# Performance work log

Hardware: AMD Instinct MI355X
Metric: run time of the kernel (lower is better)

## Reference

```python
import jax, jax.numpy as jnp
import numpy as np

H, DK, DV = 16, 128, 128
BINS = 64
EPS = 1e-6
NORM_EPS = 1e-5


def silu(x):
    return x * jax.nn.sigmoid(x)


def short_conv(x, w):
    # causal depthwise conv over time + silu. x: [B,T,C], w: [C,K]
    C = x.shape[-1]
    K = w.shape[1]
    lhs = jnp.swapaxes(x, 1, 2)              # [B,C,T]
    rhs = w[:, None, :]                      # [C,1,K]
    out = jax.lax.conv_general_dilated(
        lhs, rhs, window_strides=(1,), padding=[(K - 1, 0)],
        dimension_numbers=('NCH', 'OIH', 'NCH'), feature_group_count=C)
    return silu(jnp.swapaxes(out, 1, 2))


def delta_rule(q, k, v, beta, decay):
    # gated delta-rule linear attention recurrence.
    # q,k: [B,T,H,DK], v: [B,T,H,DV], beta: [B,T,H], decay: [B,T,H,DK]
    B = q.shape[0]

    def step(S, inp):
        qt, kt, vt, bt, gt = inp             # [B,H,DK],...,[B,H],[B,H,DK]
        Sd = S * gt[..., None]               # per-key-channel decay
        v_pred = jnp.einsum('bhk,bhkv->bhv', kt, Sd)
        S_new = Sd + jnp.einsum('bhk,bhv->bhkv', kt * bt[..., None], vt - v_pred)
        ot = jnp.einsum('bhk,bhkv->bhv', qt, S_new)
        return S_new, ot

    tm = lambda a: jnp.swapaxes(a, 0, 1)     # time-major
    S0 = jnp.zeros((B, H, DK, DV), q.dtype)
    _, o = jax.lax.scan(step, S0, (tm(q), tm(k), tm(v), tm(beta), tm(decay)))
    return jnp.swapaxes(o, 0, 1)             # [B,T,H,DV]


def _forward(hidden_states, wq, wk, wv, conv_q_w, conv_k_w, conv_v_w, A_log, dt_bias,
             proxy_w, unc_w, head_embed, mlp_w1, mlp_b1, mlp_w2, mlp_b2,
             bb_w, bb_b, bd_w, bd_b, lam_w, lam_b, ab_w, ab_b, ad_w, ad_b,
             g1_w, g2_w, g2_b, onorm_w, wo):
    x = hidden_states
    B, T, _ = x.shape
    q = short_conv(x @ wq, conv_q_w).reshape(B, T, H, DK)
    k = short_conv(x @ wk, conv_k_w).reshape(B, T, H, DK)
    v = short_conv(x @ wv, conv_v_w).reshape(B, T, H, DV)

    # uncertainty (entropy of predicted-token distribution proxy)
    logp = jax.nn.log_softmax(x @ unc_w, axis=-1)
    entropy = -jnp.sum(jnp.exp(logp) * logp, axis=-1)              # [B,T]
    ent_norm = entropy / jnp.log(jnp.asarray(BINS, x.dtype))

    # beta-norm: unit-norm keys inside the kernel
    k_unit = k / (jnp.linalg.norm(k, axis=-1, keepdims=True) + EPS)

    # proxy-value surprise features, per head/token
    v_hat = jnp.einsum('bthk,kv->bthv', k, proxy_w)
    err = v - v_hat
    err_n = jnp.linalg.norm(err, axis=-1)                          # [B,T,H]
    v_n = jnp.linalg.norm(v, axis=-1)
    vh_n = jnp.linalg.norm(v_hat, axis=-1)
    rel_err = err_n / (v_n + EPS)
    cos = jnp.sum(v * v_hat, axis=-1) / (v_n * vh_n + EPS)
    feats = jnp.stack([jnp.broadcast_to(ent_norm[..., None], err_n.shape),
                       rel_err, cos, jnp.log1p(err_n)], axis=-1)    # [B,T,H,4]
    he = jnp.broadcast_to(head_embed[None, None], (B, T, H, head_embed.shape[-1]))
    feats = jnp.concatenate([feats, he], axis=-1)                   # [B,T,H,8]

    hf = silu(silu(feats @ mlp_w1 + mlp_b1) @ mlp_w2 + mlp_b2)      # [B,T,H,32]
    beta_base = hf @ bb_w + bb_b[0]
    beta_delta = hf @ bd_w + bd_b[0]
    beta_fast = jax.nn.sigmoid(beta_base + beta_delta)              # fast memory: bigger step
    beta_slow = jax.nn.sigmoid(beta_base - beta_delta)              # slow memory: smaller step
    lam = jax.nn.sigmoid(hf @ lam_w + lam_b[0])                     # mixing gate
    amp_base = hf @ ab_w + ab_b[0]
    amp_delta = hf @ ad_w + ad_b[0]
    amp_fast = jax.nn.sigmoid(amp_base + amp_delta)
    amp_slow = jax.nn.sigmoid(amp_base - amp_delta)

    # KDA-style per-key-channel log-decay: g = -exp(A_log) * softplus(dt_bias)
    g_chan = -jnp.exp(A_log)[:, None] * jax.nn.softplus(dt_bias).reshape(H, DK)
    decay_fast = jnp.exp(g_chan[None, None] * amp_fast[..., None])  # [B,T,H,DK]
    decay_slow = jnp.exp(g_chan[None, None] * amp_slow[..., None])

    qs = q * (DK ** -0.5)
    o_fast = delta_rule(qs, k_unit, v, beta_fast, decay_fast)
    o_slow = delta_rule(qs, k_unit, v, beta_slow, decay_slow)
    o = lam[..., None] * o_fast + (1.0 - lam[..., None]) * o_slow   # [B,T,H,DV]

    # gated RMSNorm (sigmoid gate) + output projection
    g = ((x @ g1_w) @ g2_w + g2_b).reshape(B, T, H, DV)
    rms = jnp.sqrt(jnp.mean(o * o, axis=-1, keepdims=True) + NORM_EPS)
    o = (o / rms) * onorm_w * jax.nn.sigmoid(g)
    return o.reshape(B, T, H * DV) @ wo


def setup_inputs() -> dict:
    key = jax.random.key(0)
    ks = jax.random.split(key, 40)
    B, T, D = 2, 256, 2048

    def w(k, shape, fan_in):
        return jax.random.normal(k, shape, jnp.float32) * (fan_in ** -0.5)

    return {
        'hidden_states': jax.random.normal(ks[0], (B, T, D), jnp.float32),
        'wq': w(ks[1], (D, H * DK), D),
        'wk': w(ks[2], (D, H * DK), D),
        'wv': w(ks[3], (D, H * DV), D),
        'conv_q_w': w(ks[4], (H * DK, 4), 4),
        'conv_k_w': w(ks[5], (H * DK, 4), 4),
        'conv_v_w': w(ks[6], (H * DV, 4), 4),
        'A_log': jnp.log(jax.random.uniform(ks[7], (H,), jnp.float32, 1.0, 16.0)),
        'dt_bias': jnp.zeros((H * DK,), jnp.float32),
        'proxy_w': w(ks[8], (DK, DV), DK),
        'unc_w': w(ks[9], (D, BINS), D),
        'head_embed': jax.random.normal(ks[10], (H, 4), jnp.float32),
        'mlp_w1': w(ks[11], (8, 32), 8),
        'mlp_b1': jnp.zeros((32,), jnp.float32),
        'mlp_w2': w(ks[12], (32, 32), 32),
        'mlp_b2': jnp.zeros((32,), jnp.float32),
        'bb_w': w(ks[13], (32,), 32), 'bb_b': jnp.zeros((1,), jnp.float32),
        'bd_w': w(ks[14], (32,), 32), 'bd_b': jnp.zeros((1,), jnp.float32),
        'lam_w': w(ks[15], (32,), 32), 'lam_b': jnp.zeros((1,), jnp.float32),
        'ab_w': w(ks[16], (32,), 32), 'ab_b': jnp.zeros((1,), jnp.float32),
        'ad_w': w(ks[17], (32,), 32), 'ad_b': jnp.zeros((1,), jnp.float32),
        'g1_w': w(ks[18], (D, DV), D),
        'g2_w': w(ks[19], (DV, H * DV), DV),
        'g2_b': jnp.zeros((H * DV,), jnp.float32),
        'onorm_w': jnp.ones((DV,), jnp.float32),
        'wo': w(ks[20], (H * DV, D), H * DV),
    }


def reference(hidden_states, wq, wk, wv, conv_q_w, conv_k_w, conv_v_w, A_log, dt_bias,
              proxy_w, unc_w, head_embed, mlp_w1, mlp_b1, mlp_w2, mlp_b2,
              bb_w, bb_b, bd_w, bd_b, lam_w, lam_b, ab_w, ab_b, ad_w, ad_b,
              g1_w, g2_w, g2_b, onorm_w, wo):
    return _forward(hidden_states, wq, wk, wv, conv_q_w, conv_k_w, conv_v_w, A_log,
                    dt_bias, proxy_w, unc_w, head_embed, mlp_w1, mlp_b1, mlp_w2, mlp_b2,
                    bb_w, bb_b, bd_w, bd_b, lam_w, lam_b, ab_w, ab_b, ad_w, ad_b,
                    g1_w, g2_w, g2_b, onorm_w, wo)
```

## Files before the change

kernel.cpp:

```cpp
#include <hip/hip_runtime.h>
#include <hip/hip_bf16.h>
#include <math.h>

#define H_ 16
#define DK_ 128
#define DV_ 128
#define D_ 2048
#define T_ 256
#define B_ 2
#define BT_ 512

typedef __attribute__((ext_vector_type(8))) short short8v;
typedef __attribute__((ext_vector_type(4))) float float4v;
typedef unsigned short ushort_t;

__device__ __forceinline__ float sigmoidf_(float x){ return 1.f/(1.f+expf(-x)); }
__device__ __forceinline__ float siluf_(float x){ return x/(1.f+expf(-x)); }
__device__ __forceinline__ ushort_t f2bf(float f){
    __hip_bfloat16 h = __float2bfloat16(f);
    return *reinterpret_cast<ushort_t*>(&h);
}
__device__ __forceinline__ int swz(int row, int k){
    return row * 32 + ((((k >> 3) ^ (row & 3)) << 3) | (k & 7));
}

template<int CTRL>
__device__ __forceinline__ float ror_add_(float x){
    return x + __int_as_float(__builtin_amdgcn_update_dpp(
        0, __float_as_int(x), CTRL, 0xF, 0xF, true));
}
__device__ __forceinline__ float rsum16_(float x){
    x = ror_add_<0x121>(x);
    x = ror_add_<0x122>(x);
    x = ror_add_<0x124>(x);
    x = ror_add_<0x128>(x);
    return x;
}

__global__ void cvt_bf16(const float* __restrict__ in, ushort_t* __restrict__ out, int n){
    int i = (blockIdx.x * 256 + threadIdx.x) * 4;
    if (i >= n) return;
    float4 v = *(const float4*)&in[i];
    union { ushort_t s[4]; unsigned long long u; } p;
    p.s[0] = f2bf(v.x); p.s[1] = f2bf(v.y); p.s[2] = f2bf(v.z); p.s[3] = f2bf(v.w);
    *(unsigned long long*)&out[i] = p.u;
}

__global__ void cvt_strided(const float* __restrict__ Cb, ushort_t* __restrict__ out){
    int i = (blockIdx.x * 256 + threadIdx.x) * 4;
    int m = i >> 7, c = i & 127;
    float4 v = *(const float4*)&Cb[(size_t)m * 6336 + 6208 + c];
    union { ushort_t s[4]; unsigned long long u; } p;
    p.s[0] = f2bf(v.x); p.s[1] = f2bf(v.y); p.s[2] = f2bf(v.z); p.s[3] = f2bf(v.w);
    *(unsigned long long*)&out[i] = p.u;
}

__device__ __forceinline__ void gemm_core(
    const ushort_t* __restrict__ A, int K,
    const float* __restrict__ W, int Nst, int nloc0,
    float* __restrict__ C, int Cst, int m0, int n0out)
{
    __shared__ ushort_t Asub[2048];
    __shared__ ushort_t Bsub[2048];
    const int tid = threadIdx.x;
    const int wid = tid >> 6, lane = tid & 63;
    const int wr = (wid >> 1) * 32, wc = (wid & 1) * 32;
    const int lr = lane & 15, lk = (lane >> 4) * 8;
    const int rowA = tid >> 2, kqA = tid & 3;
    const int nW = tid & 63, kqW = tid >> 6;

    float4v acc[2][2];
    #pragma unroll
    for (int i = 0; i < 2; ++i)
        #pragma unroll
        for (int j = 0; j < 2; ++j) acc[i][j] = (float4v){0.f, 0.f, 0.f, 0.f};

    short8v aRa, aRb;
    float wRa[8], wRb[8];

#define LOADT(AR, WR, KOFF) do {                                                   \
    AR = *(const short8v*)&A[(size_t)(m0 + rowA) * K + (KOFF) + kqA * 8];          \
    _Pragma("unroll")                                                              \
    for (int r = 0; r < 8; ++r)                                                    \
        WR[r] = W[(size_t)((KOFF) + kqW * 8 + r) * Nst + nloc0 + nW];              \
} while (0)
#define STORET(AR, WR) do {                                                        \
    *(short8v*)&Asub[swz(rowA, kqA * 8)] = AR;                                     \
    union { ushort_t s[8]; short8v v; } pk;                                        \
    _Pragma("unroll")                                                              \
    for (int r = 0; r < 8; ++r) pk.s[r] = f2bf(WR[r]);                             \
    *(short8v*)&Bsub[swz(nW, kqW * 8)] = pk.v;                                     \
} while (0)
#define FRAGMMA() do {                                                             \
    short8v af0 = *(const short8v*)&Asub[swz(wr + lr, lk)];                        \
    short8v af1 = *(const short8v*)&Asub[swz(wr + 16 + lr, lk)];                   \
    short8v bf0 = *(const short8v*)&Bsub[swz(wc + lr, lk)];                        \
    short8v bf1 = *(const short8v*)&Bsub[swz(wc + 16 + lr, lk)];                   \
    acc[0][0] = __builtin_amdgcn_mfma_f32_16x16x32_bf16(af0, bf0, acc[0][0],0,0,0);\
    acc[0][1] = __builtin_amdgcn_mfma_f32_16x16x32_bf16(af0, bf1, acc[0][1],0,0,0);\
    acc[1][0] = __builtin_amdgcn_mfma_f32_16x16x32_bf16(af1, bf0, acc[1][0],0,0,0);\
    acc[1][1] = __builtin_amdgcn_mfma_f32_16x16x32_bf16(af1, bf1, acc[1][1],0,0,0);\
} while (0)

    LOADT(aRa, wRa, 0);
    for (int k0 = 0; k0 < K; k0 += 64) {
        STORET(aRa, wRa);
        __syncthreads();
        if (k0 + 32 < K) LOADT(aRb, wRb, k0 + 32);
        FRAGMMA();
        __syncthreads();
        STORET(aRb, wRb);
        __syncthreads();
        if (k0 + 64 < K) LOADT(aRa, wRa, k0 + 64);
        FRAGMMA();
        __syncthreads();
    }
#undef LOADT
#undef STORET
#undef FRAGMMA
    const int lq = (lane >> 4) * 4;
    #pragma unroll
    for (int mi = 0; mi < 2; ++mi)
        #pragma unroll
        for (int ni = 0; ni < 2; ++ni)
            #pragma unroll
            for (int j = 0; j < 4; ++j)
                C[(size_t)(m0 + wr + mi * 16 + lq + j) * Cst + (n0out + wc + ni * 16 + lr)]
                    = acc[mi][ni][j];
}

__device__ __forceinline__ void gemm_core2(
    const ushort_t* __restrict__ A, int K,
    const float* __restrict__ W, int Nst, int nloc0,
    float* __restrict__ C, int Cst, int m0, int n0out)
{
    __shared__ ushort_t Asub[8192];
    __shared__ ushort_t Bsub[2048];
    const int tid = threadIdx.x;
    const int wid = tid >> 6, lane = tid & 63;
    const int wr = wid * 32;
    const int lr = lane & 15, lk = (lane >> 4) * 8;
    const int rowA = tid >> 2;
    const int kqA  = (tid & 3) * 8;
    const int nW = tid & 63, kqW = (tid >> 6) & 3;
    const bool doW = tid < 256;

    float4v acc[2][4];
    #pragma unroll
    for (int i = 0; i < 2; ++i)
        #pragma unroll
        for (int j = 0; j < 4; ++j) acc[i][j] = (float4v){0.f, 0.f, 0.f, 0.f};

    short8v a0a, a1a, a0b, a1b;
    float wRa[8], wRb[8];

#define LOADT2(A0, A1, WR, KOFF) do {                                              \
    A0 = *(const short8v*)&A[(size_t)(m0 + rowA) * K + (KOFF) + kqA];              \
    A1 = *(const short8v*)&A[(size_t)(m0 + rowA + 128) * K + (KOFF) + kqA];        \
    if (doW) {                                                                     \
        _Pragma("unroll")                                                          \
        for (int r = 0; r < 8; ++r)                                                \
            WR[r] = W[(size_t)((KOFF) + kqW * 8 + r) * Nst + nloc0 + nW];          \
    }                                                                              \
} while (0)
#define STORET2(A0, A1, WR) do {                                                   \
    *(short8v*)&Asub[swz(rowA, kqA)] = A0;                                         \
    *(short8v*)&Asub[swz(rowA + 128, kqA)] = A1;                                   \
    if (doW) {                                                                     \
        union { ushort_t s[8]; short8v v; } pk;                                    \
        _Pragma("unroll")                                                          \
        for (int r = 0; r < 8; ++r) pk.s[r] = f2bf(WR[r]);                         \
        *(short8v*)&Bsub[swz(nW, kqW * 8)] = pk.v;                                 \
    }                                                                              \
} while (0)
#define FRAGMMA2() do {                                                            \
    short8v af0 = *(const short8v*)&Asub[swz(wr + lr, lk)];                        \
    short8v af1 = *(const short8v*)&Asub[swz(wr + 16 + lr, lk)];                   \
    short8v bf0 = *(const short8v*)&Bsub[swz(lr, lk)];                             \
    short8v bf1 = *(const short8v*)&Bsub[swz(16 + lr, lk)];                        \
    short8v bf2 = *(const short8v*)&Bsub[swz(32 + lr, lk)];                        \
    short8v bf3 = *(const short8v*)&Bsub[swz(48 + lr, lk)];                        \
    acc[0][0] = __builtin_amdgcn_mfma_f32_16x16x32_bf16(af0, bf0, acc[0][0],0,0,0);\
    acc[0][1] = __builtin_amdgcn_mfma_f32_16x16x32_bf16(af0, bf1, acc[0][1],0,0,0);\
    acc[0][2] = __builtin_amdgcn_mfma_f32_16x16x32_bf16(af0, bf2, acc[0][2],0,0,0);\
    acc[0][3] = __builtin_amdgcn_mfma_f32_16x16x32_bf16(af0, bf3, acc[0][3],0,0,0);\
    acc[1][0] = __builtin_amdgcn_mfma_f32_16x16x32_bf16(af1, bf0, acc[1][0],0,0,0);\
    acc[1][1] = __builtin_amdgcn_mfma_f32_16x16x32_bf16(af1, bf1, acc[1][1],0,0,0);\
    acc[1][2] = __builtin_amdgcn_mfma_f32_16x16x32_bf16(af1, bf2, acc[1][2],0,0,0);\
    acc[1][3] = __builtin_amdgcn_mfma_f32_16x16x32_bf16(af1, bf3, acc[1][3],0,0,0);\
} while (0)

    LOADT2(a0a, a1a, wRa, 0);
    for (int k0 = 0; k0 < K; k0 += 64) {
        STORET2(a0a, a1a, wRa);
        __syncthreads();
        if (k0 + 32 < K) LOADT2(a0b, a1b, wRb, k0 + 32);
        FRAGMMA2();
        __syncthreads();
        STORET2(a0b, a1b, wRb);
        __syncthreads();
        if (k0 + 64 < K) LOADT2(a0a, a1a, wRa, k0 + 64);
        FRAGMMA2();
        __syncthreads();
    }
#undef LOADT2
#undef STORET2
#undef FRAGMMA2
    const int lq = (lane >> 4) * 4;
    #pragma unroll
    for (int mi = 0; mi < 2; ++mi)
        #pragma unroll
        for (int ni = 0; ni < 4; ++ni)
            #pragma unroll
            for (int j = 0; j < 4; ++j)
                C[(size_t)(m0 + wr + mi * 16 + lq + j) * Cst + (n0out + ni * 16 + lr)]
                    = acc[mi][ni][j];
}

__global__ __launch_bounds__(512) void gemm_proj(const ushort_t* __restrict__ A,
    const float* __restrict__ wq, const float* __restrict__ wk, const float* __restrict__ wv,
    const float* __restrict__ unc, const float* __restrict__ g1, float* __restrict__ C)
{
    int n0 = blockIdx.x * 64, m0 = blockIdx.y * 256;
    const float* W; int nloc, Nst;
    if (n0 < 2048)      { W = wq;  nloc = n0;        Nst = 2048; }
    else if (n0 < 4096) { W = wk;  nloc = n0 - 2048; Nst = 2048; }
    else if (n0 < 6144) { W = wv;  nloc = n0 - 4096; Nst = 2048; }
    else if (n0 < 6208) { W = unc; nloc = n0 - 6144; Nst = 64; }
    else                { W = g1;  nloc = n0 - 6208; Nst = 128; }
    gemm_core2(A, 2048, W, Nst, nloc, C, 6336, m0, n0);
}

__global__ __launch_bounds__(256) void gemm_one(const ushort_t* __restrict__ A,
    const float* __restrict__ W, float* __restrict__ C, int N, int K)
{
    gemm_core(A, K, W, N, blockIdx.x * 64, C, N, blockIdx.y * 64, blockIdx.x * 64);
}

__global__ void conv_fused(const float* __restrict__ Cb,
    const float* __restrict__ wq, const float* __restrict__ wk, const float* __restrict__ wv,
    float* __restrict__ qc, float* __restrict__ kc, float* __restrict__ vc,
    ushort_t* __restrict__ kcb, float qscale)
{
    int c  = blockIdx.x * 256 + threadIdx.x;
    int bt = blockIdx.y;
    int b  = bt / T_, t = bt % T_;
    int which = c >> 11, cloc = c & 2047;
    const float* w = which == 0 ? wq : which == 1 ? wk : wv;
    float* o = which == 0 ? qc : which == 1 ? kc : vc;
    float scale = which == 0 ? qscale : 1.f;
    float acc = 0.f;
    #pragma unroll
    for (int j = 0; j < 4; ++j) {
        int tt = t - 3 + j;
        if (tt >= 0) acc = fmaf(w[cloc * 4 + j], Cb[((size_t)(b * T_ + tt)) * 6336 + c], acc);
    }
    float r = siluf_(acc) * scale;
    o[(size_t)bt * D_ + cloc] = r;
    if (which == 1) kcb[(size_t)bt * D_ + cloc] = f2bf(r);
}

__global__ void gchan_k(const float* __restrict__ A_log, const float* __restrict__ dt_bias,
                        float* __restrict__ gchan)
{
    int i = blockIdx.x * 256 + threadIdx.x;
    int h = i >> 7;
    float x = dt_bias[i];
    float sp = (x > 20.f) ? x : log1pf(expf(x));
    gchan[i] = -expf(A_log[h]) * sp * 1.44269504088896f;
}

__global__ __launch_bounds__(128) void feats_k(
    const float* __restrict__ kc, const float* __restrict__ vc,
    const float* __restrict__ vhatA, const float* __restrict__ Cb,
    const float* __restrict__ he,
    const float* __restrict__ w1, const float* __restrict__ b1,
    const float* __restrict__ w2, const float* __restrict__ b2,
    const float* __restrict__ bbw, const float* __restrict__ bbb,
    const float* __restrict__ bdw, const float* __restrict__ bdb,
    const float* __restrict__ lamw, const float* __restrict__ lamb,
    const float* __restrict__ abw, const float* __restrict__ abb,
    const float* __restrict__ adw, const float* __restrict__ adb,
    float* __restrict__ bf, float* __restrict__ bs, float* __restrict__ lm,
    float* __restrict__ af, float* __restrict__ as2, float* __restrict__ kn)
{
    int blk = blockIdx.x;
    int h = blk & 15, bt = blk >> 4;
    int b = bt / T_, t = bt % T_;
    int v = threadIdx.x;
    __shared__ float part[2][5];
    __shared__ float tot5[5];
    __shared__ float feats8[8];
    __shared__ float hf1[32];
    __shared__ float hf[32];
    __shared__ float entSh;

    if (v < 64) {
        float x = Cb[(size_t)bt * 6336 + 6144 + v];
        float m = x;
        #pragma unroll
        for (int o = 32; o > 0; o >>= 1) m = fmaxf(m, __shfl_xor(m, o));
        float e = expf(x - m);
        float s = e;
        #pragma unroll
        for (int o = 32; o > 0; o >>= 1) s += __shfl_xor(s, o);
        float lp = (x - m) - logf(s);
        float c = -expf(lp) * lp;
        #pragma unroll
        for (int o = 32; o > 0; o >>= 1) c += __shfl_xor(c, o);
        if (v == 0) entSh = c / logf(64.f);
    }

    size_t base = (size_t)bt * D_ + h * 128;
    float kval = kc[base + v];
    float vval = vc[base + v];
    float vhat = vhatA[(size_t)blk * 128 + v];

    float e = vval - vhat;
    float sums[5] = {kval * kval, vval * vval, vhat * vhat, vval * vhat, e * e};
    #pragma unroll
    for (int i = 0; i < 5; ++i) {
        float s = sums[i];
        #pragma unroll
        for (int o = 32; o > 0; o >>= 1) s += __shfl_xor(s, o);
        if ((threadIdx.x & 63) == 0) part[threadIdx.x >> 6][i] = s;
    }
    __syncthreads();
    if (threadIdx.x < 5) tot5[threadIdx.x] = part[0][threadIdx.x] + part[1][threadIdx.x];
    __syncthreads();
    if (threadIdx.x == 0) {
        float k2 = tot5[0], v2 = tot5[1], vh2 = tot5[2], vvh = tot5[3], e2 = tot5[4];
        float knorm = sqrtf(k2);
        float err_n = sqrtf(e2);
        float v_n = sqrtf(v2);
        float vh_n = sqrtf(vh2);
        feats8[0] = entSh;
        feats8[1] = err_n / (v_n + 1e-6f);
        feats8[2] = vvh / (v_n * vh_n + 1e-6f);
        feats8[3] = log1pf(err_n);
        feats8[4] = he[h * 4 + 0];
        feats8[5] = he[h * 4 + 1];
        feats8[6] = he[h * 4 + 2];
        feats8[7] = he[h * 4 + 3];
        kn[((size_t)(b * H_ + h)) * T_ + t] = knorm;
    }
    __syncthreads();
    if (threadIdx.x < 32) {
        float a = b1[threadIdx.x];
        #pragma unroll
        for (int j = 0; j < 8; ++j) a = fmaf(feats8[j], w1[j * 32 + threadIdx.x], a);
        hf1[threadIdx.x] = siluf_(a);
    }
    __syncthreads();
    if (threadIdx.x < 32) {
        float a = b2[threadIdx.x];
        #pragma unroll
        for (int j = 0; j < 32; ++j) a = fmaf(hf1[j], w2[j * 32 + threadIdx.x], a);
        hf[threadIdx.x] = siluf_(a);
    }
    __syncthreads();
    if (threadIdx.x == 0) {
        float bb = bbb[0], bd = bdb[0], lv = lamb[0], ab = abb[0], ad = adb[0];
        #pragma unroll
        for (int j = 0; j < 32; ++j) {
            float hj = hf[j];
            bb = fmaf(hj, bbw[j], bb);
            bd = fmaf(hj, bdw[j], bd);
            lv = fmaf(hj, lamw[j], lv);
            ab = fmaf(hj, abw[j], ab);
            ad = fmaf(hj, adw[j], ad);
        }
        size_t o = ((size_t)(b * H_ + h)) * T_ + t;
        bf[o]  = sigmoidf_(bb + bd);
        bs[o]  = sigmoidf_(bb - bd);
        lm[o]  = sigmoidf_(lv);
        af[o]  = sigmoidf_(ab + ad);
        as2[o] = sigmoidf_(ab - ad);
    }
}

__global__ __launch_bounds__(128) void precomp_k(
    const float* __restrict__ kc, const float* __restrict__ qc,
    const float* __restrict__ kn,
    const float* __restrict__ af, const float* __restrict__ as2,
    const float* __restrict__ bf, const float* __restrict__ bs,
    const float* __restrict__ gchan,
    float* __restrict__ kuA, float* __restrict__ dA, float4* __restrict__ scal4A)
{
    const int t = blockIdx.x;
    const int y = blockIdx.y;
    const int rule = y >> 5, b = (y >> 4) & 1, h = y & 15;
    const int k = threadIdx.x;
    const int sb = (b * 16 + h) * 256 + t;
    const float knv = kn[sb];
    const float am  = (rule ? as2 : af)[sb];
    const float btv = (rule ? bs : bf)[sb];
    const size_t idx = (size_t)(b * 256 + t) * D_ + h * 128 + k;
    const float kuv = kc[idx] / (knv + 1e-6f);
    if (rule == 0) kuA[((size_t)(b * 16 + h) * 256 + t) * 128 + k] = kuv;
    dA[((size_t)y * 256 + t) * 128 + k] = exp2f(gchan[h * 128 + k] * am);
    float p = qc[idx] * kuv;
    #pragma unroll
    for (int o = 32; o > 0; o >>= 1) p += __shfl_xor(p, o);
    __shared__ float pp[2];
    if ((k & 63) == 0) pp[k >> 6] = p;
    __syncthreads();
    if (k == 0) {
        float4 s; s.x = am; s.y = btv; s.z = (pp[0] + pp[1]) * btv; s.w = 0.f;
        scal4A[(size_t)y * 256 + t] = s;
    }
}

struct OPS { float4 a0, a1, q0, q1, d0, d1, sc; float2 vv; };

__global__ __launch_bounds__(256) void delta_wave9(
    const float* __restrict__ qc, const float* __restrict__ vc,
    const float* __restrict__ kuA, const float* __restrict__ dA,
    const float4* __restrict__ scal4A,
    float* __restrict__ o_fast, float* __restrict__ o_slow)
{
    const int p  = blockIdx.x;
    const int lb = (p & 7) * 32 + (p >> 3);
    const int bh = lb >> 3, rule = (lb >> 2) & 1, vq = lb & 3;
    const int b = bh >> 4, h = bh & 15;
    const int rbh = rule * 32 + bh;
    const int tid = threadIdx.x;
    const int wid = tid >> 6, lane = tid & 63;
    const int kl = lane & 15, vg = lane >> 4;
    const int vloc = wid * 8 + vg * 2;
    const int vcol = vq * 32 + vloc;

    __shared__ float kuL[2][16][144];
    __shared__ float qL [2][16][144];
    __shared__ float dL [2][16][144];
    __shared__ float vL [2][16][32];
    __shared__ float scL[2][16][4];

    const float*  __restrict__ pkuG = kuA + (size_t)bh * 256 * 128;
    const float*  __restrict__ pdG  = dA + (size_t)rbh * 256 * 128;
    const float*  __restrict__ pqG  = qc + (size_t)b * T_ * D_ + h * 128;
    const float*  __restrict__ pvG  = vc + (size_t)b * T_ * D_ + h * 128 + vq * 32;
    const float4* __restrict__ pscG = scal4A + (size_t)rbh * 256;
    float* __restrict__ obase = (rule ? o_slow : o_fast)
                                + (size_t)b * T_ * D_ + h * 128 + vcol;

    const int srow = (tid & 127) >> 3;
    const int scol = (tid & 7) * 16;
    const bool isK = tid < 128;
    const int ck0 = scol >> 3;
    const int fo_w0 = ck0 * 8 + (ck0 >> 2) * 4;
    const int fo_w1 = (ck0 + 1) * 8 + ((ck0 + 1) >> 2) * 4;

    float4 sb0, sb1, sb2, sb3, svb, ssc, sd0, sd1;

    float S[8][2];
    #pragma unroll
    for (int j = 0; j < 8; ++j) { S[j][0] = 0.f; S[j][1] = 0.f; }

#define STAGE_LOAD(C) do {                                                         \
    const int t0_ = (C) * 16;                                                      \
    const float* dsrc = pdG + (size_t)(t0_ + srow) * 128 + scol;                   \
    if (isK) {                                                                     \
        const float* src = pkuG + (size_t)(t0_ + srow) * 128 + scol;               \
        sb0 = *(const float4*)(src);      sb1 = *(const float4*)(src + 4);         \
        sb2 = *(const float4*)(src + 8);  sb3 = *(const float4*)(src + 12);        \
        svb = *(const float4*)(pvG + (size_t)(t0_ + srow) * D_ + (tid & 7) * 4);   \
        sd0 = *(const float4*)(dsrc);     sd1 = *(const float4*)(dsrc + 4);        \
    } else {                                                                       \
        const float* src = pqG + (size_t)(t0_ + srow) * D_ + scol;                 \
        sb0 = *(const float4*)(src);      sb1 = *(const float4*)(src + 4);         \
        sb2 = *(const float4*)(src + 8);  sb3 = *(const float4*)(src + 12);        \
        sd0 = *(const float4*)(dsrc + 8); sd1 = *(const float4*)(dsrc + 12);       \
        if ((tid & 127) < 16) ssc = *(const float4*)&pscG[t0_ + (tid & 127)];      \
    }                                                                              \
} while (0)

#define STAGE_WRITE(BI) do {                                                       \
    if (isK) {                                                                     \
        *(float4*)&kuL[BI][srow][fo_w0]     = sb0;                                 \
        *(float4*)&kuL[BI][srow][fo_w0 + 4] = sb1;                                 \
        *(float4*)&kuL[BI][srow][fo_w1]     = sb2;                                 \
        *(float4*)&kuL[BI][srow][fo_w1 + 4] = sb3;                                 \
        *(float4*)&vL[BI][srow][(tid & 7) * 4] = svb;                              \
        *(float4*)&dL[BI][srow][fo_w0]      = sd0;                                 \
        *(float4*)&dL[BI][srow][fo_w0 + 4]  = sd1;                                 \
    } else {                                                                       \
        *(float4*)&qL[BI][srow][fo_w0]     = sb0;                                  \
        *(float4*)&qL[BI][srow][fo_w0 + 4] = sb1;                                  \
        *(float4*)&qL[BI][srow][fo_w1]     = sb2;                                  \
        *(float4*)&qL[BI][srow][fo_w1 + 4] = sb3;                                  \
        *(float4*)&dL[BI][srow][fo_w1]      = sd0;                                 \
        *(float4*)&dL[BI][srow][fo_w1 + 4]  = sd1;                                 \
        if ((tid & 127) < 16) *(float4*)&scL[BI][tid & 127][0] = ssc;              \
    }                                                                              \
} while (0)

#define LDOPS(R, BI, TS) do {                                                      \
    R.a0 = *(const float4*)&kuL[BI][TS][fo];                                       \
    R.a1 = *(const float4*)&kuL[BI][TS][fo + 4];                                   \
    R.q0 = *(const float4*)&qL[BI][TS][fo];                                        \
    R.q1 = *(const float4*)&qL[BI][TS][fo + 4];                                    \
    R.d0 = *(const float4*)&dL[BI][TS][fo];                                        \
    R.d1 = *(const float4*)&dL[BI][TS][fo + 4];                                    \
    R.vv = *(const float2*)&vL[BI][TS][vloc];                                      \
    R.sc = *(const float4*)&scL[BI][TS][0];                                        \
} while (0)

#define STEP(TT, CUR, NXT, BI) do {                                                \
    if ((TT) + 1 < 16) LDOPS(NXT, BI, (TT) + 1);                                   \
    float ku[8] = {CUR.a0.x, CUR.a0.y, CUR.a0.z, CUR.a0.w,                         \
                   CUR.a1.x, CUR.a1.y, CUR.a1.z, CUR.a1.w};                        \
    float qv[8] = {CUR.q0.x, CUR.q0.y, CUR.q0.z, CUR.q0.w,                         \
                   CUR.q1.x, CUR.q1.y, CUR.q1.z, CUR.q1.w};                        \
    float d[8]  = {CUR.d0.x, CUR.d0.y, CUR.d0.z, CUR.d0.w,                         \
                   CUR.d1.x, CUR.d1.y, CUR.d1.z, CUR.d1.w};                        \
    float vp0a = 0.f, vp0b = 0.f, vp1a = 0.f, vp1b = 0.f;                          \
    float oq0a = 0.f, oq0b = 0.f, oq1a = 0.f, oq1b = 0.f;                          \
    _Pragma("unroll")                                                              \
    for (int j = 0; j < 4; ++j) {                                                  \
        float kudA = ku[j] * d[j],     qdA = qv[j] * d[j];                         \
        float kudB = ku[j+4] * d[j+4], qdB = qv[j+4] * d[j+4];                     \
        vp0a = fmaf(kudA, S[j][0], vp0a);   vp0b = fmaf(kudB, S[j+4][0], vp0b);    \
        vp1a = fmaf(kudA, S[j][1], vp1a);   vp1b = fmaf(kudB, S[j+4][1], vp1b);    \
        oq0a = fmaf(qdA,  S[j][0], oq0a);   oq0b = fmaf(qdB,  S[j+4][0], oq0b);    \
        oq1a = fmaf(qdA,  S[j][1], oq1a);   oq1b = fmaf(qdB,  S[j+4][1], oq1b);    \
    }                                                                              \
    float vp0 = rsum16_(vp0a + vp0b);                                              \
    float vp1 = rsum16_(vp1a + vp1b);                                              \
    float oq0 = rsum16_(oq0a + oq0b);                                              \
    float oq1 = rsum16_(oq1a + oq1b);                                              \
    float dv0 = CUR.vv.x - vp0, dv1 = CUR.vv.y - vp1;                              \
    float o0 = fmaf(CUR.sc.z, dv0, oq0);                                           \
    float o1 = fmaf(CUR.sc.z, dv1, oq1);                                           \
    float bd0 = CUR.sc.y * dv0, bd1 = CUR.sc.y * dv1;                              \
    _Pragma("unroll")                                                              \
    for (int j = 0; j < 8; ++j) {                                                  \
        S[j][0] = fmaf(d[j], S[j][0], ku[j] * bd0);                                \
        S[j][1] = fmaf(d[j], S[j][1], ku[j] * bd1);                                \
    }                                                                              \
    if (kl == 0) {                                                                 \
        float2 ov; ov.x = o0; ov.y = o1;                                           \
        *(float2*)&obase[(size_t)(tb + (TT)) * D_] = ov;                           \
    }                                                                              \
} while (0)

    const int fo = kl * 8 + (kl >> 2) * 4;

    STAGE_LOAD(0);
    STAGE_WRITE(0);
    __syncthreads();

    OPS rA, rB;
    for (int c = 0; c < 16; ++c) {
        if (c < 15) STAGE_LOAD(c + 1);
        const int bi = c & 1;
        const int tb = c * 16;
        LDOPS(rA, bi, 0);
        #pragma unroll
        for (int ts = 0; ts < 16; ts += 2) {
            STEP(ts,     rA, rB, bi);
            STEP(ts + 1, rB, rA, bi);
        }
        if (c < 15) STAGE_WRITE((c + 1) & 1);
        __syncthreads();
    }
#undef STAGE_LOAD
#undef STAGE_WRITE
#undef LDOPS
#undef STEP
}

__global__ __launch_bounds__(128) void combine_k(
    const float* __restrict__ of, const float* __restrict__ os,
    const float* __restrict__ lm, const float* __restrict__ graw,
    const float* __restrict__ g2b, const float* __restrict__ onw,
    ushort_t* __restrict__ ocb)
{
    int blk = blockIdx.x;
    int h = blk & 15, bt = blk >> 4;
    int b = bt / T_, t = bt % T_;
    int v = threadIdx.x;
    size_t idx = (size_t)bt * D_ + h * 128 + v;
    float l = lm[((size_t)(b * H_ + h)) * T_ + t];
    float o = l * of[idx] + (1.f - l) * os[idx];
    float s = o * o;
    #pragma unroll
    for (int off = 32; off > 0; off >>= 1) s += __shfl_xor(s, off);
    __shared__ float ws2[2];
    if ((threadIdx.x & 63) == 0) ws2[threadIdx.x >> 6] = s;
    __syncthreads();
    float tot = ws2[0] + ws2[1];
    float rms = sqrtf(tot / 128.f + 1e-5f);
    float g = graw[idx] + g2b[h * 128 + v];
    ocb[idx] = f2bf(o / rms * onw[v] * sigmoidf_(g));
}

extern "C" void kernel_launch(void* const* d_in, const int* in_sizes, int n_in,
                              void* d_out, int out_size, void* d_ws, size_t ws_size,
                              hipStream_t stream)
{
    const float* x        = (const float*)d_in[0];
    const float* wq       = (const float*)d_in[1];
    const float* wk       = (const float*)d_in[2];
    const float* wv       = (const float*)d_in[3];
    const float* conv_q_w = (const float*)d_in[4];
    const float* conv_k_w = (const float*)d_in[5];
    const float* conv_v_w = (const float*)d_in[6];
    const float* A_log    = (const float*)d_in[7];
    const float* dt_bias  = (const float*)d_in[8];
    const float* proxy_w  = (const float*)d_in[9];
    const float* unc_w    = (const float*)d_in[10];
    const float* he       = (const float*)d_in[11];
    const float* mlp_w1   = (const float*)d_in[12];
    const float* mlp_b1   = (const float*)d_in[13];
    const float* mlp_w2   = (const float*)d_in[14];
    const float* mlp_b2   = (const float*)d_in[15];
    const float* bb_w     = (const float*)d_in[16];
    const float* bb_b     = (const float*)d_in[17];
    const float* bd_w     = (const float*)d_in[18];
    const float* bd_b     = (const float*)d_in[19];
    const float* lam_w    = (const float*)d_in[20];
    const float* lam_b    = (const float*)d_in[21];
    const float* ab_w     = (const float*)d_in[22];
    const float* ab_b     = (const float*)d_in[23];
    const float* ad_w     = (const float*)d_in[24];
    const float* ad_b     = (const float*)d_in[25];
    const float* g1_w     = (const float*)d_in[26];
    const float* g2_w     = (const float*)d_in[27];
    const float* g2_b     = (const float*)d_in[28];
    const float* onorm_w  = (const float*)d_in[29];
    const float* wo       = (const float*)d_in[30];
    float* out = (float*)d_out;

    float* ws = (float*)d_ws;
    const size_t SZ = (size_t)BT_ * D_;
    float* C_big = ws;
    float* qc    = C_big + (size_t)512 * 6336;
    float* kc    = qc + SZ;
    float* vc    = kc + SZ;
    float* graw  = vc + SZ;
    float* bf    = graw + SZ;
    float* bs    = bf + 8192;
    float* lm    = bs + 8192;
    float* af    = lm + 8192;
    float* as2   = af + 8192;
    float* kn    = as2 + 8192;
    float* gchan = kn + 8192;
    float* scal4 = gchan + 2048;
    float* kuA   = scal4 + 65536;
    float* dA    = kuA + 1048576;
    float* fend  = dA + 2097152;
    ushort_t* xb    = (ushort_t*)fend;
    ushort_t* gtmpb = xb + SZ;

    float* o_fast  = C_big;
    float* o_slow  = C_big + SZ;
    ushort_t* ocb  = xb;
    float* vhatA   = kuA;
    ushort_t* kcb  = (ushort_t*)dA;

    dim3 blk256(256);
    dim3 blk512(512);
    const float QSCALE = 0.08838834764831845f;

    cvt_bf16<<<dim3(1024), blk256, 0, stream>>>(x, xb, (int)SZ);
    gemm_proj<<<dim3(99, 2), blk512, 0, stream>>>(xb, wq, wk, wv, unc_w, g1_w, C_big);
    cvt_strided<<<dim3(64), blk256, 0, stream>>>(C_big, gtmpb);
    gemm_one<<<dim3(32, 8), blk256, 0, stream>>>(gtmpb, g2_w, graw, 2048, 128);
    conv_fused<<<dim3(24, BT_), blk256, 0, stream>>>(C_big, conv_q_w, conv_k_w, conv_v_w,
                                                     qc, kc, vc, kcb, QSCALE);
    gemm_one<<<dim3(2, 128), blk256, 0, stream>>>(kcb, proxy_w, vhatA, 128, 128);
    gchan_k<<<dim3(8), blk256, 0, stream>>>(A_log, dt_bias, gchan);
    feats_k<<<dim3(BT_ * H_), dim3(128), 0, stream>>>(
        kc, vc, vhatA, C_big, he, mlp_w1, mlp_b1, mlp_w2, mlp_b2,
        bb_w, bb_b, bd_w, bd_b, lam_w, lam_b, ab_w, ab_b, ad_w, ad_b,
        bf, bs, lm, af, as2, kn);
    precomp_k<<<dim3(256, 64), dim3(128), 0, stream>>>(
        kc, qc, kn, af, as2, bf, bs, gchan, kuA, dA, (float4*)scal4);
    delta_wave9<<<dim3(256), blk256, 0, stream>>>(qc, vc, kuA, dA,
                                                  (const float4*)scal4,
                                                  o_fast, o_slow);
    combine_k<<<dim3(BT_ * H_), dim3(128), 0, stream>>>(o_fast, o_slow, lm, graw,
                                                        g2_b, onorm_w, ocb);
    gemm_one<<<dim3(32, 8), blk256, 0, stream>>>(ocb, wo, out, 2048, 2048);
}
```

Measured before the change: 219.1 us.

## Fuse feature, gate-channel and precompute kernels; fold g2 conversion into GEMM

Merges gchan_k, feats_k and precomp_k into one per-(token,head) kernel that computes the gating scalars in shared memory and directly writes kuA, both decay arrays and the scal4 entries. This drops the intermediate bf/bs/af/as2/kn buffers and two launches. The g2 GEMM now reads the fp32 slice of C_big and converts it to bf16 in its loader, which removes the cvt_strided pass. The output projection moves to the larger 512-thread gemm_core2 tile. In exchange, the merged kernel recomputes the softplus gate per block, and the bigger output tiles launch only 64 blocks.

```diff
diff --git a/kernel.cpp b/kernel.cpp
--- a/kernel.cpp
+++ b/kernel.cpp
@@ -41,15 +41,6 @@
     int i = (blockIdx.x * 256 + threadIdx.x) * 4;
     if (i >= n) return;
     float4 v = *(const float4*)&in[i];
-    union { ushort_t s[4]; unsigned long long u; } p;
-    p.s[0] = f2bf(v.x); p.s[1] = f2bf(v.y); p.s[2] = f2bf(v.z); p.s[3] = f2bf(v.w);
-    *(unsigned long long*)&out[i] = p.u;
-}
-
-__global__ void cvt_strided(const float* __restrict__ Cb, ushort_t* __restrict__ out){
-    int i = (blockIdx.x * 256 + threadIdx.x) * 4;
-    int m = i >> 7, c = i & 127;
-    float4 v = *(const float4*)&Cb[(size_t)m * 6336 + 6208 + c];
     union { ushort_t s[4]; unsigned long long u; } p;
     p.s[0] = f2bf(v.x); p.s[1] = f2bf(v.y); p.s[2] = f2bf(v.z); p.s[3] = f2bf(v.w);
     *(unsigned long long*)&out[i] = p.u;
@@ -237,6 +228,68 @@
     gemm_core(A, K, W, N, blockIdx.x * 64, C, N, blockIdx.y * 64, blockIdx.x * 64);
 }
 
+__global__ __launch_bounds__(512) void gemm_one2(const ushort_t* __restrict__ A,
+    const float* __restrict__ W, float* __restrict__ C, int N, int K)
+{
+    gemm_core2(A, K, W, N, blockIdx.x * 64, C, N, blockIdx.y * 256, blockIdx.x * 64);
+}
+
+__global__ __launch_bounds__(256) void gemm_g2(const float* __restrict__ Cb,
+    const float* __restrict__ W, float* __restrict__ C)
+{
+    __shared__ ushort_t Asub[2048];
+    __shared__ ushort_t Bsub[2048];
+    const int tid = threadIdx.x;
+    const int wid = tid >> 6, lane = tid & 63;
+    const int wr = (wid >> 1) * 32, wc = (wid & 1) * 32;
+    const int lr = lane & 15, lk = (lane >> 4) * 8;
+    const int rowA = tid >> 2, kqA = (tid & 3) * 8;
+    const int nW = tid & 63, kqW = tid >> 6;
+    const int m0 = blockIdx.y * 64, n0 = blockIdx.x * 64;
+
+    float4v acc[2][2];
+    #pragma unroll
+    for (int i = 0; i < 2; ++i)
+        #pragma unroll
+        for (int j = 0; j < 2; ++j) acc[i][j] = (float4v){0.f, 0.f, 0.f, 0.f};
+
+    for (int k0 = 0; k0 < 128; k0 += 32) {
+        const float* asrc = &Cb[(size_t)(m0 + rowA) * 6336 + 6208 + k0 + kqA];
+        float4 a4a = *(const float4*)asrc;
+        float4 a4b = *(const float4*)(asrc + 4);
+        float w8[8];
+        #pragma unroll
+        for (int r = 0; r < 8; ++r)
+            w8[r] = W[(size_t)(k0 + kqW * 8 + r) * 2048 + n0 + nW];
+        __syncthreads();
+        union { ushort_t s[8]; short8v v; } pa, pw;
+        pa.s[0]=f2bf(a4a.x); pa.s[1]=f2bf(a4a.y); pa.s[2]=f2bf(a4a.z); pa.s[3]=f2bf(a4a.w);
+        pa.s[4]=f2bf(a4b.x); pa.s[5]=f2bf(a4b.y); pa.s[6]=f2bf(a4b.z); pa.s[7]=f2bf(a4b.w);
+        *(short8v*)&Asub[swz(rowA, kqA)] = pa.v;
+        #pragma unroll
+        for (int r = 0; r < 8; ++r) pw.s[r] = f2bf(w8[r]);
+        *(short8v*)&Bsub[swz(nW, kqW * 8)] = pw.v;
+        __syncthreads();
+        short8v af0 = *(const short8v*)&Asub[swz(wr + lr, lk)];
+        short8v af1 = *(const short8v*)&Asub[swz(wr + 16 + lr, lk)];
+        short8v bf0 = *(const short8v*)&Bsub[swz(wc + lr, lk)];
+        short8v bf1 = *(const short8v*)&Bsub[swz(wc + 16 + lr, lk)];
+        acc[0][0] = __builtin_amdgcn_mfma_f32_16x16x32_bf16(af0, bf0, acc[0][0],0,0,0);
+        acc[0][1] = __builtin_amdgcn_mfma_f32_16x16x32_bf16(af0, bf1, acc[0][1],0,0,0);
+        acc[1][0] = __builtin_amdgcn_mfma_f32_16x16x32_bf16(af1, bf0, acc[1][0],0,0,0);
+        acc[1][1] = __builtin_amdgcn_mfma_f32_16x16x32_bf16(af1, bf1, acc[1][1],0,0,0);
+    }
+    const int lq = (lane >> 4) * 4;
+    #pragma unroll
+    for (int mi = 0; mi < 2; ++mi)
+        #pragma unroll
+        for (int ni = 0; ni < 2; ++ni)
+            #pragma unroll
+            for (int j = 0; j < 4; ++j)
+                C[(size_t)(m0 + wr + mi * 16 + lq + j) * 2048 + (n0 + wc + ni * 16 + lr)]
+                    = acc[mi][ni][j];
+}
+
 __global__ void conv_fused(const float* __restrict__ Cb,
     const float* __restrict__ wq, const float* __restrict__ wk, const float* __restrict__ wv,
     float* __restrict__ qc, float* __restrict__ kc, float* __restrict__ vc,
@@ -260,20 +313,12 @@
     if (which == 1) kcb[(size_t)bt * D_ + cloc] = f2bf(r);
 }
 
-__global__ void gchan_k(const float* __restrict__ A_log, const float* __restrict__ dt_bias,
-                        float* __restrict__ gchan)
-{
-    int i = blockIdx.x * 256 + threadIdx.x;
-    int h = i >> 7;
-    float x = dt_bias[i];
-    float sp = (x > 20.f) ? x : log1pf(expf(x));
-    gchan[i] = -expf(A_log[h]) * sp * 1.44269504088896f;
-}
-
-__global__ __launch_bounds__(128) void feats_k(
+__global__ __launch_bounds__(128) void featsprec_k(
     const float* __restrict__ kc, const float* __restrict__ vc,
+    const float* __restrict__ qc,
     const float* __restrict__ vhatA, const float* __restrict__ Cb,
     const float* __restrict__ he,
+    const float* __restrict__ A_log, const float* __restrict__ dt_bias,
     const float* __restrict__ w1, const float* __restrict__ b1,
     const float* __restrict__ w2, const float* __restrict__ b2,
     const float* __restrict__ bbw, const float* __restrict__ bbb,
@@ -281,8 +326,8 @@
     const float* __restrict__ lamw, const float* __restrict__ lamb,
     const float* __restrict__ abw, const float* __restrict__ abb,
     const float* __restrict__ adw, const float* __restrict__ adb,
-    float* __restrict__ bf, float* __restrict__ bs, float* __restrict__ lm,
-    float* __restrict__ af, float* __restrict__ as2, float* __restrict__ kn)
+    float* __restrict__ lm, float* __restrict__ kuA,
+    float* __restrict__ dA, float4* __restrict__ scal4A)
 {
     int blk = blockIdx.x;
     int h = blk & 15, bt = blk >> 4;
@@ -294,6 +339,7 @@
     __shared__ float hf1[32];
     __shared__ float hf[32];
     __shared__ float entSh;
+    __shared__ float scal5[5];
 
     if (v < 64) {
         float x = Cb[(size_t)bt * 6336 + 6144 + v];
@@ -342,7 +388,7 @@
         feats8[5] = he[h * 4 + 1];
         feats8[6] = he[h * 4 + 2];
         feats8[7] = he[h * 4 + 3];
-        kn[((size_t)(b * H_ + h)) * T_ + t] = knorm;
+        scal5[4] = knorm;
     }
     __syncthreads();
     if (threadIdx.x < 32) {
@@ -370,44 +416,36 @@
             ab = fmaf(hj, abw[j], ab);
             ad = fmaf(hj, adw[j], ad);
         }
-        size_t o = ((size_t)(b * H_ + h)) * T_ + t;
-        bf[o]  = sigmoidf_(bb + bd);
-        bs[o]  = sigmoidf_(bb - bd);
-        lm[o]  = sigmoidf_(lv);
-        af[o]  = sigmoidf_(ab + ad);
-        as2[o] = sigmoidf_(ab - ad);
-    }
-}
-
-__global__ __launch_bounds__(128) void precomp_k(
-    const float* __restrict__ kc, const float* __restrict__ qc,
-    const float* __restrict__ kn,
-    const float* __restrict__ af, const float* __restrict__ as2,
-    const float* __restrict__ bf, const float* __restrict__ bs,
-    const float* __restrict__ gchan,
-    float* __restrict__ kuA, float* __restrict__ dA, float4* __restrict__ scal4A)
-{
-    const int t = blockIdx.x;
-    const int y = blockIdx.y;
-    const int rule = y >> 5, b = (y >> 4) & 1, h = y & 15;
+        scal5[0] = sigmoidf_(bb + bd);
+        scal5[1] = sigmoidf_(bb - bd);
+        scal5[2] = sigmoidf_(ab + ad);
+        scal5[3] = sigmoidf_(ab - ad);
+        lm[((size_t)(b * H_ + h)) * T_ + t] = sigmoidf_(lv);
+    }
+    __syncthreads();
+
+    const float bfv = scal5[0], bsv = scal5[1];
+    const float afv = scal5[2], asv = scal5[3], knv = scal5[4];
     const int k = threadIdx.x;
-    const int sb = (b * 16 + h) * 256 + t;
-    const float knv = kn[sb];
-    const float am  = (rule ? as2 : af)[sb];
-    const float btv = (rule ? bs : bf)[sb];
-    const size_t idx = (size_t)(b * 256 + t) * D_ + h * 128 + k;
-    const float kuv = kc[idx] / (knv + 1e-6f);
-    if (rule == 0) kuA[((size_t)(b * 16 + h) * 256 + t) * 128 + k] = kuv;
-    dA[((size_t)y * 256 + t) * 128 + k] = exp2f(gchan[h * 128 + k] * am);
-    float p = qc[idx] * kuv;
-    #pragma unroll
-    for (int o = 32; o > 0; o >>= 1) p += __shfl_xor(p, o);
-    __shared__ float pp[2];
-    if ((k & 63) == 0) pp[k >> 6] = p;
-    __syncthreads();
-    if (k == 0) {
-        float4 s; s.x = am; s.y = btv; s.z = (pp[0] + pp[1]) * btv; s.w = 0.f;
-        scal4A[(size_t)y * 256 + t] = s;
+    const int bh = b * 16 + h;
+    float xdt = dt_bias[h * 128 + k];
+    float sp = (xdt > 20.f) ? xdt : log1pf(expf(xdt));
+    float gch = -expf(A_log[h]) * sp * 1.44269504088896f;
+    float kuv = kval / (knv + 1e-6f);
+    kuA[((size_t)bh * 256 + t) * 128 + k] = kuv;
+    dA[((size_t)bh * 256 + t) * 128 + k]        = exp2f(gch * afv);
+    dA[((size_t)(32 + bh) * 256 + t) * 128 + k] = exp2f(gch * asv);
+    float pq = qc[base + k] * kuv;
+    #pragma unroll
+    for (int o = 32; o > 0; o >>= 1) pq += __shfl_xor(pq, o);
+    if ((threadIdx.x & 63) == 0) part[threadIdx.x >> 6][0] = pq;
+    __syncthreads();
+    if (threadIdx.x == 0) {
+        float pt = part[0][0] + part[1][0];
+        float4 s0; s0.x = afv; s0.y = bfv; s0.z = pt * bfv; s0.w = 0.f;
+        float4 s1; s1.x = asv; s1.y = bsv; s1.z = pt * bsv; s1.w = 0.f;
+        scal4A[(size_t)bh * 256 + t] = s0;
+        scal4A[(size_t)(32 + bh) * 256 + t] = s1;
     }
 }
 
@@ -639,24 +677,17 @@
     float* kc    = qc + SZ;
     float* vc    = kc + SZ;
     float* graw  = vc + SZ;
-    float* bf    = graw + SZ;
-    float* bs    = bf + 8192;
-    float* lm    = bs + 8192;
-    float* af    = lm + 8192;
-    float* as2   = af + 8192;
-    float* kn    = as2 + 8192;
-    float* gchan = kn + 8192;
-    float* scal4 = gchan + 2048;
+    float* lm    = graw + SZ;
+    float* scal4 = lm + 8192;
     float* kuA   = scal4 + 65536;
     float* dA    = kuA + 1048576;
-    float* fend  = dA + 2097152;
-    ushort_t* xb    = (ushort_t*)fend;
-    ushort_t* gtmpb = xb + SZ;
+    float* vhatA = dA + 2097152;
+    float* fend  = vhatA + 1048576;
+    ushort_t* xb = (ushort_t*)fend;
 
     float* o_fast  = C_big;
     float* o_slow  = C_big + SZ;
     ushort_t* ocb  = xb;
-    float* vhatA   = kuA;
     ushort_t* kcb  = (ushort_t*)dA;
 
     dim3 blk256(256);
@@ -665,22 +696,19 @@
 
     cvt_bf16<<<dim3(1024), blk256, 0, stream>>>(x, xb, (int)SZ);
     gemm_proj<<<dim3(99, 2), blk512, 0, stream>>>(xb, wq, wk, wv, unc_w, g1_w, C_big);
-    cvt_strided<<<dim3(64), blk256, 0, stream>>>(C_big, gtmpb);
-    gemm_one<<<dim3(32, 8), blk256, 0, stream>>>(gtmpb, g2_w, graw, 2048, 128);
+    gemm_g2<<<dim3(32, 8), blk256, 0, stream>>>(C_big, g2_w, graw);
     conv_fused<<<dim3(24, BT_), blk256, 0, stream>>>(C_big, conv_q_w, conv_k_w, conv_v_w,
                                                      qc, kc, vc, kcb, QSCALE);
     gemm_one<<<dim3(2, 128), blk256, 0, stream>>>(kcb, proxy_w, vhatA, 128, 128);
-    gchan_k<<<dim3(8), blk256, 0, stream>>>(A_log, dt_bias, gchan);
-    feats_k<<<dim3(BT_ * H_), dim3(128), 0, stream>>>(
-        kc, vc, vhatA, C_big, he, mlp_w1, mlp_b1, mlp_w2, mlp_b2,
+    featsprec_k<<<dim3(BT_ * H_), dim3(128), 0, stream>>>(
+        kc, vc, qc, vhatA, C_big, he, A_log, dt_bias,
+        mlp_w1, mlp_b1, mlp_w2, mlp_b2,
         bb_w, bb_b, bd_w, bd_b, lam_w, lam_b, ab_w, ab_b, ad_w, ad_b,
-        bf, bs, lm, af, as2, kn);
-    precomp_k<<<dim3(256, 64), dim3(128), 0, stream>>>(
-        kc, qc, kn, af, as2, bf, bs, gchan, kuA, dA, (float4*)scal4);
+        lm, kuA, dA, (float4*)scal4);
     delta_wave9<<<dim3(256), blk256, 0, stream>>>(qc, vc, kuA, dA,
                                                   (const float4*)scal4,
                                                   o_fast, o_slow);
     combine_k<<<dim3(BT_ * H_), dim3(128), 0, stream>>>(o_fast, o_slow, lm, graw,
                                                         g2_b, onorm_w, ocb);
-    gemm_one<<<dim3(32, 8), blk256, 0, stream>>>(ocb, wo, out, 2048, 2048);
-}
+    gemm_one2<<<dim3(32, 2), blk512, 0, stream>>>(ocb, wo, out, 2048, 2048);
+}
```

Result: slower. 223.8 us (+2.2%).
